# Optimization experiments

Measured on AMD Instinct MI355X. Metric: run time of the kernel, lower is better.

## Reference

```python
import jax, jax.numpy as jnp
import numpy as np

N = 100000
E = 6400000
D = 512


def setup_inputs() -> dict:
    key = jax.random.key(0)
    k1, k2, k3, k4 = jax.random.split(key, 4)
    x = jax.random.normal(k1, (N, D), dtype=jnp.float32)
    edge_index = jax.random.randint(k2, (2, E), 0, N, dtype=jnp.int64)
    edge_attr = jax.random.uniform(k3, (E,), dtype=jnp.float32)
    # xavier_normal_ on (in_feat, 1) with gain=1.414: std = gain*sqrt(2/(fan_in+fan_out))
    std = 1.414 * np.sqrt(2.0 / (D + 1))
    p = jax.random.normal(k4, (D, 1), dtype=jnp.float32) * std
    b = jnp.zeros((1,), dtype=jnp.float32)
    return {"x": x, "edge_index": edge_index, "edge_attr": edge_attr, "p": p, "b": b}


def reference(x, edge_index, edge_attr, p, b):
    # Per-node gate: sigmoid(x @ p + b), shape [N]
    diag_val = jax.nn.sigmoid(jnp.matmul(x, p) + b).reshape(-1)
    # spspmm(A, diag(d)) scales each edge value by d[col] = d[edge_index[1]]
    adj_mat_val = edge_attr * diag_val[edge_index[1]]
    return edge_index, adj_mat_val
```

## Files before the change

kernel.cpp:

```cpp
#include <hip/hip_runtime.h>
#include <math.h>


typedef float vf4 __attribute__((ext_vector_type(4)));
typedef int   vi4 __attribute__((ext_vector_type(4)));

__global__ __launch_bounds__(256) void gate_kernel(
    const float* __restrict__ x,
    const float* __restrict__ p,
    const float* __restrict__ b,
    float* __restrict__ gate,
    int N)
{
    const int wave_id = (blockIdx.x * blockDim.x + threadIdx.x) >> 6;
    const int lane    = threadIdx.x & 63;
    const float bb = b[0];

    const vf4* pr = (const vf4*)p;
    const vf4 p0 = pr[lane];
    const vf4 p1 = pr[lane + 64];

    const int row0 = wave_id * 4;
    if (row0 >= N) return;

    if (row0 + 3 < N) {
        const vf4* xr = (const vf4*)(x + (size_t)row0 * 512);
        vf4 a0 = __builtin_nontemporal_load(xr + lane);
        vf4 a1 = __builtin_nontemporal_load(xr + lane + 64);
        vf4 b0 = __builtin_nontemporal_load(xr + lane + 128);
        vf4 b1 = __builtin_nontemporal_load(xr + lane + 192);
        vf4 c0 = __builtin_nontemporal_load(xr + lane + 256);
        vf4 c1 = __builtin_nontemporal_load(xr + lane + 320);
        vf4 d0 = __builtin_nontemporal_load(xr + lane + 384);
        vf4 d1 = __builtin_nontemporal_load(xr + lane + 448);

        float s0 = a0.x * p0.x + a0.y * p0.y + a0.z * p0.z + a0.w * p0.w
                 + a1.x * p1.x + a1.y * p1.y + a1.z * p1.z + a1.w * p1.w;
        float s1 = b0.x * p0.x + b0.y * p0.y + b0.z * p0.z + b0.w * p0.w
                 + b1.x * p1.x + b1.y * p1.y + b1.z * p1.z + b1.w * p1.w;
        float s2 = c0.x * p0.x + c0.y * p0.y + c0.z * p0.z + c0.w * p0.w
                 + c1.x * p1.x + c1.y * p1.y + c1.z * p1.z + c1.w * p1.w;
        float s3 = d0.x * p0.x + d0.y * p0.y + d0.z * p0.z + d0.w * p0.w
                 + d1.x * p1.x + d1.y * p1.y + d1.z * p1.z + d1.w * p1.w;

        #pragma unroll
        for (int off = 32; off > 0; off >>= 1) {
            s0 += __shfl_down(s0, off, 64);
            s1 += __shfl_down(s1, off, 64);
            s2 += __shfl_down(s2, off, 64);
            s3 += __shfl_down(s3, off, 64);
        }
        if (lane == 0) {
            vf4 g;
            g.x = 1.0f / (1.0f + __expf(-(s0 + bb)));
            g.y = 1.0f / (1.0f + __expf(-(s1 + bb)));
            g.z = 1.0f / (1.0f + __expf(-(s2 + bb)));
            g.w = 1.0f / (1.0f + __expf(-(s3 + bb)));
            *(vf4*)(gate + row0) = g;
        }
    } else {
        for (int row = row0; row < N; ++row) {
            const vf4* xr = (const vf4*)(x + (size_t)row * 512);
            vf4 x0 = xr[lane];
            vf4 x1 = xr[lane + 64];
            float s = x0.x * p0.x + x0.y * p0.y + x0.z * p0.z + x0.w * p0.w
                    + x1.x * p1.x + x1.y * p1.y + x1.z * p1.z + x1.w * p1.w;
            #pragma unroll
            for (int off = 32; off > 0; off >>= 1)
                s += __shfl_down(s, off, 64);
            if (lane == 0)
                gate[row] = 1.0f / (1.0f + __expf(-(s + bb)));
        }
    }
}

__global__ __launch_bounds__(256) void edge_kernel(
    const int*   __restrict__ edge_index,
    const float* __restrict__ edge_attr,
    const float* __restrict__ gate,
    float* __restrict__ out,
    int E)
{
    const int tid = blockIdx.x * blockDim.x + threadIdx.x;
    const int EV4 = E >> 2;
    const int q0  = tid * 2;
    if (q0 >= EV4) return;

    const vi4* row4 = (const vi4*)edge_index;
    const vi4* col4 = (const vi4*)(edge_index + E);
    const vf4* ea4  = (const vf4*)edge_attr;

    vf4* outR = (vf4*)out;
    vf4* outC = (vf4*)(out + (size_t)E);
    vf4* outV = (vf4*)(out + 2 * (size_t)E);

    vi4 c0 = __builtin_nontemporal_load(col4 + q0);
    vi4 c1 = __builtin_nontemporal_load(col4 + q0 + 1);
    vi4 r0 = __builtin_nontemporal_load(row4 + q0);
    vi4 r1 = __builtin_nontemporal_load(row4 + q0 + 1);
    vf4 a0 = __builtin_nontemporal_load(ea4 + q0);
    vf4 a1 = __builtin_nontemporal_load(ea4 + q0 + 1);

    float g0x = gate[c0.x], g0y = gate[c0.y], g0z = gate[c0.z], g0w = gate[c0.w];
    float g1x = gate[c1.x], g1y = gate[c1.y], g1z = gate[c1.z], g1w = gate[c1.w];

    vf4 fr0; fr0.x = (float)r0.x; fr0.y = (float)r0.y; fr0.z = (float)r0.z; fr0.w = (float)r0.w;
    vf4 fr1; fr1.x = (float)r1.x; fr1.y = (float)r1.y; fr1.z = (float)r1.z; fr1.w = (float)r1.w;
    vf4 fc0; fc0.x = (float)c0.x; fc0.y = (float)c0.y; fc0.z = (float)c0.z; fc0.w = (float)c0.w;
    vf4 fc1; fc1.x = (float)c1.x; fc1.y = (float)c1.y; fc1.z = (float)c1.z; fc1.w = (float)c1.w;

    __builtin_nontemporal_store(fr0, outR + q0);
    __builtin_nontemporal_store(fr1, outR + q0 + 1);
    __builtin_nontemporal_store(fc0, outC + q0);
    __builtin_nontemporal_store(fc1, outC + q0 + 1);

    vf4 v0, v1;
    v0.x = a0.x * g0x;  v0.y = a0.y * g0y;  v0.z = a0.z * g0z;  v0.w = a0.w * g0w;
    v1.x = a1.x * g1x;  v1.y = a1.y * g1y;  v1.z = a1.z * g1z;  v1.w = a1.w * g1w;
    __builtin_nontemporal_store(v0, outV + q0);
    __builtin_nontemporal_store(v1, outV + q0 + 1);
}

extern "C" void kernel_launch(void* const* d_in, const int* in_sizes, int n_in,
                              void* d_out, int out_size, void* d_ws, size_t ws_size,
                              hipStream_t stream) {
    const float* x          = (const float*)d_in[0];
    const int*   edge_index = (const int*)  d_in[1];
    const float* edge_attr  = (const float*)d_in[2];
    const float* p          = (const float*)d_in[3];
    const float* b          = (const float*)d_in[4];

    const int D = in_sizes[3];
    const int N = in_sizes[0] / D;
    const int E = in_sizes[2];

    float* gate = (float*)d_ws;
    float* out  = (float*)d_out;

    int gate_waves  = (N + 3) / 4;
    int gate_blocks = (gate_waves + 3) / 4;
    gate_kernel<<<gate_blocks, 256, 0, stream>>>(x, p, b, gate, N);

    int edge_threads = (E >> 2) / 2;
    int edge_blocks  = (edge_threads + 255) / 256;
    edge_kernel<<<edge_blocks, 256, 0, stream>>>(edge_index, edge_attr, gate, out, E);
}
```

Before: 351.3 us.

## Fuse gate and edge kernels into one cooperative kernel with grid sync

```diff
diff --git a/kernel.cpp b/kernel.cpp
--- a/kernel.cpp
+++ b/kernel.cpp
@@ -1,28 +1,145 @@
 #include <hip/hip_runtime.h>
+#include <hip/hip_cooperative_groups.h>
 #include <math.h>
+
+namespace cg = cooperative_groups;
 
 
 typedef float vf4 __attribute__((ext_vector_type(4)));
 typedef int   vi4 __attribute__((ext_vector_type(4)));
 
-__global__ __launch_bounds__(256) void gate_kernel(
+#define COOP_BLOCKS 1024
+#define COOP_THREADS 256
+
+__global__ __launch_bounds__(256, 4) void fused_kernel(
     const float* __restrict__ x,
+    const int*   __restrict__ edge_index,
+    const float* __restrict__ edge_attr,
     const float* __restrict__ p,
     const float* __restrict__ b,
     float* __restrict__ gate,
-    int N)
+    float* __restrict__ out,
+    int N, int E)
+{
+    const int tid     = blockIdx.x * blockDim.x + threadIdx.x;
+    const int nthread = gridDim.x * blockDim.x;
+    const int wave_id = tid >> 6;
+    const int lane    = threadIdx.x & 63;
+    const int nwaves  = nthread >> 6;
+
+    const int EV4 = E >> 2;
+
+    {
+        const vi4* row4 = (const vi4*)edge_index;
+        vf4*       outR = (vf4*)out;
+        for (int i = tid; i < EV4; i += nthread) {
+            vi4 r = __builtin_nontemporal_load(row4 + i);
+            vf4 fr;
+            fr.x = (float)r.x; fr.y = (float)r.y;
+            fr.z = (float)r.z; fr.w = (float)r.w;
+            __builtin_nontemporal_store(fr, outR + i);
+        }
+    }
+
+    {
+        const float bb = b[0];
+        const vf4* pr = (const vf4*)p;
+        const vf4 p0 = pr[lane];
+        const vf4 p1 = pr[lane + 64];
+        const int ntask = (N + 3) >> 2;
+
+        for (int t = wave_id; t < ntask; t += nwaves) {
+            const int row0 = t * 4;
+            if (row0 + 3 < N) {
+                const vf4* xr = (const vf4*)(x + (size_t)row0 * 512);
+                vf4 a0 = __builtin_nontemporal_load(xr + lane);
+                vf4 a1 = __builtin_nontemporal_load(xr + lane + 64);
+                vf4 b0 = __builtin_nontemporal_load(xr + lane + 128);
+                vf4 b1 = __builtin_nontemporal_load(xr + lane + 192);
+                vf4 c0 = __builtin_nontemporal_load(xr + lane + 256);
+                vf4 c1 = __builtin_nontemporal_load(xr + lane + 320);
+                vf4 d0 = __builtin_nontemporal_load(xr + lane + 384);
+                vf4 d1 = __builtin_nontemporal_load(xr + lane + 448);
+
+                float s0 = a0.x*p0.x + a0.y*p0.y + a0.z*p0.z + a0.w*p0.w
+                         + a1.x*p1.x + a1.y*p1.y + a1.z*p1.z + a1.w*p1.w;
+                float s1 = b0.x*p0.x + b0.y*p0.y + b0.z*p0.z + b0.w*p0.w
+                         + b1.x*p1.x + b1.y*p1.y + b1.z*p1.z + b1.w*p1.w;
+                float s2 = c0.x*p0.x + c0.y*p0.y + c0.z*p0.z + c0.w*p0.w
+                         + c1.x*p1.x + c1.y*p1.y + c1.z*p1.z + c1.w*p1.w;
+                float s3 = d0.x*p0.x + d0.y*p0.y + d0.z*p0.z + d0.w*p0.w
+                         + d1.x*p1.x + d1.y*p1.y + d1.z*p1.z + d1.w*p1.w;
+
+                #pragma unroll
+                for (int off = 32; off > 0; off >>= 1) {
+                    s0 += __shfl_down(s0, off, 64);
+                    s1 += __shfl_down(s1, off, 64);
+                    s2 += __shfl_down(s2, off, 64);
+                    s3 += __shfl_down(s3, off, 64);
+                }
+                if (lane == 0) {
+                    vf4 g;
+                    g.x = 1.0f / (1.0f + __expf(-(s0 + bb)));
+                    g.y = 1.0f / (1.0f + __expf(-(s1 + bb)));
+                    g.z = 1.0f / (1.0f + __expf(-(s2 + bb)));
+                    g.w = 1.0f / (1.0f + __expf(-(s3 + bb)));
+                    *(vf4*)(gate + row0) = g;
+                }
+            } else {
+                for (int row = row0; row < N; ++row) {
+                    const vf4* xr = (const vf4*)(x + (size_t)row * 512);
+                    vf4 x0 = xr[lane];
+                    vf4 x1 = xr[lane + 64];
+                    float s = x0.x*p0.x + x0.y*p0.y + x0.z*p0.z + x0.w*p0.w
+                            + x1.x*p1.x + x1.y*p1.y + x1.z*p1.z + x1.w*p1.w;
+                    #pragma unroll
+                    for (int off = 32; off > 0; off >>= 1)
+                        s += __shfl_down(s, off, 64);
+                    if (lane == 0)
+                        gate[row] = 1.0f / (1.0f + __expf(-(s + bb)));
+                }
+            }
+        }
+    }
+
+    cg::this_grid().sync();
+
+    {
+        const vi4* col4 = (const vi4*)(edge_index + E);
+        const vf4* ea4  = (const vf4*)edge_attr;
+        vf4* outC = (vf4*)(out + (size_t)E);
+        vf4* outV = (vf4*)(out + 2 * (size_t)E);
+
+        for (int i = tid; i < EV4; i += nthread) {
+            vi4 c = __builtin_nontemporal_load(col4 + i);
+            vf4 a = __builtin_nontemporal_load(ea4 + i);
+
+            float gx = gate[c.x], gy = gate[c.y], gz = gate[c.z], gw = gate[c.w];
+
+            vf4 fc;
+            fc.x = (float)c.x; fc.y = (float)c.y;
+            fc.z = (float)c.z; fc.w = (float)c.w;
+            __builtin_nontemporal_store(fc, outC + i);
+
+            vf4 v;
+            v.x = a.x * gx; v.y = a.y * gy; v.z = a.z * gz; v.w = a.w * gw;
+            __builtin_nontemporal_store(v, outV + i);
+        }
+    }
+}
+
+__global__ __launch_bounds__(256) void gate_kernel(
+    const float* __restrict__ x, const float* __restrict__ p,
+    const float* __restrict__ b, float* __restrict__ gate, int N)
 {
     const int wave_id = (blockIdx.x * blockDim.x + threadIdx.x) >> 6;
     const int lane    = threadIdx.x & 63;
     const float bb = b[0];
-
     const vf4* pr = (const vf4*)p;
     const vf4 p0 = pr[lane];
     const vf4 p1 = pr[lane + 64];
-
     const int row0 = wave_id * 4;
     if (row0 >= N) return;
-
     if (row0 + 3 < N) {
         const vf4* xr = (const vf4*)(x + (size_t)row0 * 512);
         vf4 a0 = __builtin_nontemporal_load(xr + lane);
@@ -33,16 +150,14 @@
         vf4 c1 = __builtin_nontemporal_load(xr + lane + 320);
         vf4 d0 = __builtin_nontemporal_load(xr + lane + 384);
         vf4 d1 = __builtin_nontemporal_load(xr + lane + 448);
-
-        float s0 = a0.x * p0.x + a0.y * p0.y + a0.z * p0.z + a0.w * p0.w
-                 + a1.x * p1.x + a1.y * p1.y + a1.z * p1.z + a1.w * p1.w;
-        float s1 = b0.x * p0.x + b0.y * p0.y + b0.z * p0.z + b0.w * p0.w
-                 + b1.x * p1.x + b1.y * p1.y + b1.z * p1.z + b1.w * p1.w;
-        float s2 = c0.x * p0.x + c0.y * p0.y + c0.z * p0.z + c0.w * p0.w
-                 + c1.x * p1.x + c1.y * p1.y + c1.z * p1.z + c1.w * p1.w;
-        float s3 = d0.x * p0.x + d0.y * p0.y + d0.z * p0.z + d0.w * p0.w
-                 + d1.x * p1.x + d1.y * p1.y + d1.z * p1.z + d1.w * p1.w;
-
+        float s0 = a0.x*p0.x + a0.y*p0.y + a0.z*p0.z + a0.w*p0.w
+                 + a1.x*p1.x + a1.y*p1.y + a1.z*p1.z + a1.w*p1.w;
+        float s1 = b0.x*p0.x + b0.y*p0.y + b0.z*p0.z + b0.w*p0.w
+                 + b1.x*p1.x + b1.y*p1.y + b1.z*p1.z + b1.w*p1.w;
+        float s2 = c0.x*p0.x + c0.y*p0.y + c0.z*p0.z + c0.w*p0.w
+                 + c1.x*p1.x + c1.y*p1.y + c1.z*p1.z + c1.w*p1.w;
+        float s3 = d0.x*p0.x + d0.y*p0.y + d0.z*p0.z + d0.w*p0.w
+                 + d1.x*p1.x + d1.y*p1.y + d1.z*p1.z + d1.w*p1.w;
         #pragma unroll
         for (int off = 32; off > 0; off >>= 1) {
             s0 += __shfl_down(s0, off, 64);
@@ -63,8 +178,8 @@
             const vf4* xr = (const vf4*)(x + (size_t)row * 512);
             vf4 x0 = xr[lane];
             vf4 x1 = xr[lane + 64];
-            float s = x0.x * p0.x + x0.y * p0.y + x0.z * p0.z + x0.w * p0.w
-                    + x1.x * p1.x + x1.y * p1.y + x1.z * p1.z + x1.w * p1.w;
+            float s = x0.x*p0.x + x0.y*p0.y + x0.z*p0.z + x0.w*p0.w
+                    + x1.x*p1.x + x1.y*p1.y + x1.z*p1.z + x1.w*p1.w;
             #pragma unroll
             for (int off = 32; off > 0; off >>= 1)
                 s += __shfl_down(s, off, 64);
@@ -75,48 +190,38 @@
 }
 
 __global__ __launch_bounds__(256) void edge_kernel(
-    const int*   __restrict__ edge_index,
-    const float* __restrict__ edge_attr,
-    const float* __restrict__ gate,
-    float* __restrict__ out,
-    int E)
+    const int* __restrict__ edge_index, const float* __restrict__ edge_attr,
+    const float* __restrict__ gate, float* __restrict__ out, int E)
 {
     const int tid = blockIdx.x * blockDim.x + threadIdx.x;
     const int EV4 = E >> 2;
     const int q0  = tid * 2;
     if (q0 >= EV4) return;
-
     const vi4* row4 = (const vi4*)edge_index;
     const vi4* col4 = (const vi4*)(edge_index + E);
     const vf4* ea4  = (const vf4*)edge_attr;
-
     vf4* outR = (vf4*)out;
     vf4* outC = (vf4*)(out + (size_t)E);
     vf4* outV = (vf4*)(out + 2 * (size_t)E);
-
     vi4 c0 = __builtin_nontemporal_load(col4 + q0);
     vi4 c1 = __builtin_nontemporal_load(col4 + q0 + 1);
     vi4 r0 = __builtin_nontemporal_load(row4 + q0);
     vi4 r1 = __builtin_nontemporal_load(row4 + q0 + 1);
     vf4 a0 = __builtin_nontemporal_load(ea4 + q0);
     vf4 a1 = __builtin_nontemporal_load(ea4 + q0 + 1);
-
     float g0x = gate[c0.x], g0y = gate[c0.y], g0z = gate[c0.z], g0w = gate[c0.w];
     float g1x = gate[c1.x], g1y = gate[c1.y], g1z = gate[c1.z], g1w = gate[c1.w];
-
-    vf4 fr0; fr0.x = (float)r0.x; fr0.y = (float)r0.y; fr0.z = (float)r0.z; fr0.w = (float)r0.w;
-    vf4 fr1; fr1.x = (float)r1.x; fr1.y = (float)r1.y; fr1.z = (float)r1.z; fr1.w = (float)r1.w;
-    vf4 fc0; fc0.x = (float)c0.x; fc0.y = (float)c0.y; fc0.z = (float)c0.z; fc0.w = (float)c0.w;
-    vf4 fc1; fc1.x = (float)c1.x; fc1.y = (float)c1.y; fc1.z = (float)c1.z; fc1.w = (float)c1.w;
-
+    vf4 fr0; fr0.x=(float)r0.x; fr0.y=(float)r0.y; fr0.z=(float)r0.z; fr0.w=(float)r0.w;
+    vf4 fr1; fr1.x=(float)r1.x; fr1.y=(float)r1.y; fr1.z=(float)r1.z; fr1.w=(float)r1.w;
+    vf4 fc0; fc0.x=(float)c0.x; fc0.y=(float)c0.y; fc0.z=(float)c0.z; fc0.w=(float)c0.w;
+    vf4 fc1; fc1.x=(float)c1.x; fc1.y=(float)c1.y; fc1.z=(float)c1.z; fc1.w=(float)c1.w;
     __builtin_nontemporal_store(fr0, outR + q0);
     __builtin_nontemporal_store(fr1, outR + q0 + 1);
     __builtin_nontemporal_store(fc0, outC + q0);
     __builtin_nontemporal_store(fc1, outC + q0 + 1);
-
     vf4 v0, v1;
-    v0.x = a0.x * g0x;  v0.y = a0.y * g0y;  v0.z = a0.z * g0z;  v0.w = a0.w * g0w;
-    v1.x = a1.x * g1x;  v1.y = a1.y * g1y;  v1.z = a1.z * g1z;  v1.w = a1.w * g1w;
+    v0.x = a0.x*g0x; v0.y = a0.y*g0y; v0.z = a0.z*g0z; v0.w = a0.w*g0w;
+    v1.x = a1.x*g1x; v1.y = a1.y*g1y; v1.z = a1.z*g1z; v1.w = a1.w*g1w;
     __builtin_nontemporal_store(v0, outV + q0);
     __builtin_nontemporal_store(v1, outV + q0 + 1);
 }
@@ -131,17 +236,25 @@
     const float* b          = (const float*)d_in[4];
 
     const int D = in_sizes[3];
-    const int N = in_sizes[0] / D;
-    const int E = in_sizes[2];
+    int N = in_sizes[0] / D;
+    int E = in_sizes[2];
 
     float* gate = (float*)d_ws;
     float* out  = (float*)d_out;
 
-    int gate_waves  = (N + 3) / 4;
-    int gate_blocks = (gate_waves + 3) / 4;
-    gate_kernel<<<gate_blocks, 256, 0, stream>>>(x, p, b, gate, N);
-
-    int edge_threads = (E >> 2) / 2;
-    int edge_blocks  = (edge_threads + 255) / 256;
-    edge_kernel<<<edge_blocks, 256, 0, stream>>>(edge_index, edge_attr, gate, out, E);
-}
+    void* args[] = {(void*)&x, (void*)&edge_index, (void*)&edge_attr,
+                    (void*)&p, (void*)&b, (void*)&gate, (void*)&out,
+                    (void*)&N, (void*)&E};
+    hipError_t err = hipLaunchCooperativeKernel(
+        (const void*)fused_kernel, dim3(COOP_BLOCKS), dim3(COOP_THREADS),
+        args, 0, stream);
+
+    if (err != hipSuccess) {
+        int gate_waves  = (N + 3) / 4;
+        int gate_blocks = (gate_waves + 3) / 4;
+        gate_kernel<<<gate_blocks, 256, 0, stream>>>(x, p, b, gate, N);
+        int edge_threads = (E >> 2) / 2;
+        int edge_blocks  = (edge_threads + 255) / 256;
+        edge_kernel<<<edge_blocks, 256, 0, stream>>>(edge_index, edge_attr, gate, out, E);
+    }
+}
```

Result: slower. 487.1 us (+38.6%).

## Move row-index conversion into gate kernel to overlap with gate GEMV

Applied to the files above, without the earlier changes.

```diff
diff --git a/kernel.cpp b/kernel.cpp
--- a/kernel.cpp
+++ b/kernel.cpp
@@ -5,72 +5,94 @@
 typedef float vf4 __attribute__((ext_vector_type(4)));
 typedef int   vi4 __attribute__((ext_vector_type(4)));
 
-__global__ __launch_bounds__(256) void gate_kernel(
+__global__ __launch_bounds__(256) void gate_rowconv_kernel(
     const float* __restrict__ x,
+    const int*   __restrict__ edge_index,
     const float* __restrict__ p,
     const float* __restrict__ b,
     float* __restrict__ gate,
-    int N)
+    float* __restrict__ out,
+    int N, int E, int gate_blocks)
 {
-    const int wave_id = (blockIdx.x * blockDim.x + threadIdx.x) >> 6;
-    const int lane    = threadIdx.x & 63;
-    const float bb = b[0];
+    if ((int)blockIdx.x < gate_blocks) {
+        const int wave_id = (blockIdx.x * blockDim.x + threadIdx.x) >> 6;
+        const int lane    = threadIdx.x & 63;
+        const float bb = b[0];
 
-    const vf4* pr = (const vf4*)p;
-    const vf4 p0 = pr[lane];
-    const vf4 p1 = pr[lane + 64];
+        const vf4* pr = (const vf4*)p;
+        const vf4 p0 = pr[lane];
+        const vf4 p1 = pr[lane + 64];
 
-    const int row0 = wave_id * 4;
-    if (row0 >= N) return;
+        const int row0 = wave_id * 4;
+        if (row0 >= N) return;
 
-    if (row0 + 3 < N) {
-        const vf4* xr = (const vf4*)(x + (size_t)row0 * 512);
-        vf4 a0 = __builtin_nontemporal_load(xr + lane);
-        vf4 a1 = __builtin_nontemporal_load(xr + lane + 64);
-        vf4 b0 = __builtin_nontemporal_load(xr + lane + 128);
-        vf4 b1 = __builtin_nontemporal_load(xr + lane + 192);
-        vf4 c0 = __builtin_nontemporal_load(xr + lane + 256);
-        vf4 c1 = __builtin_nontemporal_load(xr + lane + 320);
-        vf4 d0 = __builtin_nontemporal_load(xr + lane + 384);
-        vf4 d1 = __builtin_nontemporal_load(xr + lane + 448);
+        if (row0 + 3 < N) {
+            const vf4* xr = (const vf4*)(x + (size_t)row0 * 512);
+            vf4 a0 = __builtin_nontemporal_load(xr + lane);
+            vf4 a1 = __builtin_nontemporal_load(xr + lane + 64);
+            vf4 b0 = __builtin_nontemporal_load(xr + lane + 128);
+            vf4 b1 = __builtin_nontemporal_load(xr + lane + 192);
+            vf4 c0 = __builtin_nontemporal_load(xr + lane + 256);
+            vf4 c1 = __builtin_nontemporal_load(xr + lane + 320);
+            vf4 d0 = __builtin_nontemporal_load(xr + lane + 384);
+            vf4 d1 = __builtin_nontemporal_load(xr + lane + 448);
 
-        float s0 = a0.x * p0.x + a0.y * p0.y + a0.z * p0.z + a0.w * p0.w
-                 + a1.x * p1.x + a1.y * p1.y + a1.z * p1.z + a1.w * p1.w;
-        float s1 = b0.x * p0.x + b0.y * p0.y + b0.z * p0.z + b0.w * p0.w
-                 + b1.x * p1.x + b1.y * p1.y + b1.z * p1.z + b1.w * p1.w;
-        float s2 = c0.x * p0.x + c0.y * p0.y + c0.z * p0.z + c0.w * p0.w
-                 + c1.x * p1.x + c1.y * p1.y + c1.z * p1.z + c1.w * p1.w;
-        float s3 = d0.x * p0.x + d0.y * p0.y + d0.z * p0.z + d0.w * p0.w
-                 + d1.x * p1.x + d1.y * p1.y + d1.z * p1.z + d1.w * p1.w;
+            float s0 = a0.x*p0.x + a0.y*p0.y + a0.z*p0.z + a0.w*p0.w
+                     + a1.x*p1.x + a1.y*p1.y + a1.z*p1.z + a1.w*p1.w;
+            float s1 = b0.x*p0.x + b0.y*p0.y + b0.z*p0.z + b0.w*p0.w
+                     + b1.x*p1.x + b1.y*p1.y + b1.z*p1.z + b1.w*p1.w;
+            float s2 = c0.x*p0.x + c0.y*p0.y + c0.z*p0.z + c0.w*p0.w
+                     + c1.x*p1.x + c1.y*p1.y + c1.z*p1.z + c1.w*p1.w;
+            float s3 = d0.x*p0.x + d0.y*p0.y + d0.z*p0.z + d0.w*p0.w
+                     + d1.x*p1.x + d1.y*p1.y + d1.z*p1.z + d1.w*p1.w;
 
-        #pragma unroll
-        for (int off = 32; off > 0; off >>= 1) {
-            s0 += __shfl_down(s0, off, 64);
-            s1 += __shfl_down(s1, off, 64);
-            s2 += __shfl_down(s2, off, 64);
-            s3 += __shfl_down(s3, off, 64);
-        }
-        if (lane == 0) {
-            vf4 g;
-            g.x = 1.0f / (1.0f + __expf(-(s0 + bb)));
-            g.y = 1.0f / (1.0f + __expf(-(s1 + bb)));
-            g.z = 1.0f / (1.0f + __expf(-(s2 + bb)));
-            g.w = 1.0f / (1.0f + __expf(-(s3 + bb)));
-            *(vf4*)(gate + row0) = g;
+            #pragma unroll
+            for (int off = 32; off > 0; off >>= 1) {
+                s0 += __shfl_down(s0, off, 64);
+                s1 += __shfl_down(s1, off, 64);
+                s2 += __shfl_down(s2, off, 64);
+                s3 += __shfl_down(s3, off, 64);
+            }
+            if (lane == 0) {
+                vf4 g;
+                g.x = 1.0f / (1.0f + __expf(-(s0 + bb)));
+                g.y = 1.0f / (1.0f + __expf(-(s1 + bb)));
+                g.z = 1.0f / (1.0f + __expf(-(s2 + bb)));
+                g.w = 1.0f / (1.0f + __expf(-(s3 + bb)));
+                *(vf4*)(gate + row0) = g;
+            }
+        } else {
+            for (int row = row0; row < N; ++row) {
+                const vf4* xr = (const vf4*)(x + (size_t)row * 512);
+                vf4 x0 = xr[lane];
+                vf4 x1 = xr[lane + 64];
+                float s = x0.x*p0.x + x0.y*p0.y + x0.z*p0.z + x0.w*p0.w
+                        + x1.x*p1.x + x1.y*p1.y + x1.z*p1.z + x1.w*p1.w;
+                #pragma unroll
+                for (int off = 32; off > 0; off >>= 1)
+                    s += __shfl_down(s, off, 64);
+                if (lane == 0)
+                    gate[row] = 1.0f / (1.0f + __expf(-(s + bb)));
+            }
         }
     } else {
-        for (int row = row0; row < N; ++row) {
-            const vf4* xr = (const vf4*)(x + (size_t)row * 512);
-            vf4 x0 = xr[lane];
-            vf4 x1 = xr[lane + 64];
-            float s = x0.x * p0.x + x0.y * p0.y + x0.z * p0.z + x0.w * p0.w
-                    + x1.x * p1.x + x1.y * p1.y + x1.z * p1.z + x1.w * p1.w;
-            #pragma unroll
-            for (int off = 32; off > 0; off >>= 1)
-                s += __shfl_down(s, off, 64);
-            if (lane == 0)
-                gate[row] = 1.0f / (1.0f + __expf(-(s + bb)));
-        }
+        const int tid = ((int)blockIdx.x - gate_blocks) * blockDim.x + threadIdx.x;
+        const int EV4 = E >> 2;
+        const int q0  = tid * 2;
+        if (q0 >= EV4) return;
+
+        const vi4* row4 = (const vi4*)edge_index;
+        vf4*       outR = (vf4*)out;
+
+        vi4 r0 = __builtin_nontemporal_load(row4 + q0);
+        vi4 r1 = __builtin_nontemporal_load(row4 + q0 + 1);
+
+        vf4 fr0; fr0.x=(float)r0.x; fr0.y=(float)r0.y; fr0.z=(float)r0.z; fr0.w=(float)r0.w;
+        vf4 fr1; fr1.x=(float)r1.x; fr1.y=(float)r1.y; fr1.z=(float)r1.z; fr1.w=(float)r1.w;
+
+        __builtin_nontemporal_store(fr0, outR + q0);
+        if (q0 + 1 < EV4)
+            __builtin_nontemporal_store(fr1, outR + q0 + 1);
     }
 }
 
@@ -86,37 +108,29 @@
     const int q0  = tid * 2;
     if (q0 >= EV4) return;
 
-    const vi4* row4 = (const vi4*)edge_index;
     const vi4* col4 = (const vi4*)(edge_index + E);
     const vf4* ea4  = (const vf4*)edge_attr;
 
-    vf4* outR = (vf4*)out;
     vf4* outC = (vf4*)(out + (size_t)E);
     vf4* outV = (vf4*)(out + 2 * (size_t)E);
 
     vi4 c0 = __builtin_nontemporal_load(col4 + q0);
     vi4 c1 = __builtin_nontemporal_load(col4 + q0 + 1);
-    vi4 r0 = __builtin_nontemporal_load(row4 + q0);
-    vi4 r1 = __builtin_nontemporal_load(row4 + q0 + 1);
     vf4 a0 = __builtin_nontemporal_load(ea4 + q0);
     vf4 a1 = __builtin_nontemporal_load(ea4 + q0 + 1);
 
     float g0x = gate[c0.x], g0y = gate[c0.y], g0z = gate[c0.z], g0w = gate[c0.w];
     float g1x = gate[c1.x], g1y = gate[c1.y], g1z = gate[c1.z], g1w = gate[c1.w];
 
-    vf4 fr0; fr0.x = (float)r0.x; fr0.y = (float)r0.y; fr0.z = (float)r0.z; fr0.w = (float)r0.w;
-    vf4 fr1; fr1.x = (float)r1.x; fr1.y = (float)r1.y; fr1.z = (float)r1.z; fr1.w = (float)r1.w;
-    vf4 fc0; fc0.x = (float)c0.x; fc0.y = (float)c0.y; fc0.z = (float)c0.z; fc0.w = (float)c0.w;
-    vf4 fc1; fc1.x = (float)c1.x; fc1.y = (float)c1.y; fc1.z = (float)c1.z; fc1.w = (float)c1.w;
+    vf4 fc0; fc0.x=(float)c0.x; fc0.y=(float)c0.y; fc0.z=(float)c0.z; fc0.w=(float)c0.w;
+    vf4 fc1; fc1.x=(float)c1.x; fc1.y=(float)c1.y; fc1.z=(float)c1.z; fc1.w=(float)c1.w;
 
-    __builtin_nontemporal_store(fr0, outR + q0);
-    __builtin_nontemporal_store(fr1, outR + q0 + 1);
     __builtin_nontemporal_store(fc0, outC + q0);
     __builtin_nontemporal_store(fc1, outC + q0 + 1);
 
     vf4 v0, v1;
-    v0.x = a0.x * g0x;  v0.y = a0.y * g0y;  v0.z = a0.z * g0z;  v0.w = a0.w * g0w;
-    v1.x = a1.x * g1x;  v1.y = a1.y * g1y;  v1.z = a1.z * g1z;  v1.w = a1.w * g1w;
+    v0.x = a0.x*g0x; v0.y = a0.y*g0y; v0.z = a0.z*g0z; v0.w = a0.w*g0w;
+    v1.x = a1.x*g1x; v1.y = a1.y*g1y; v1.z = a1.z*g1z; v1.w = a1.w*g1w;
     __builtin_nontemporal_store(v0, outV + q0);
     __builtin_nontemporal_store(v1, outV + q0 + 1);
 }
@@ -131,17 +145,20 @@
     const float* b          = (const float*)d_in[4];
 
     const int D = in_sizes[3];
-    const int N = in_sizes[0] / D;
-    const int E = in_sizes[2];
+    int N = in_sizes[0] / D;
+    int E = in_sizes[2];
 
     float* gate = (float*)d_ws;
     float* out  = (float*)d_out;
 
     int gate_waves  = (N + 3) / 4;
     int gate_blocks = (gate_waves + 3) / 4;
-    gate_kernel<<<gate_blocks, 256, 0, stream>>>(x, p, b, gate, N);
+    int conv_threads = ((E >> 2) + 1) / 2;
+    int conv_blocks  = (conv_threads + 255) / 256;
+    gate_rowconv_kernel<<<gate_blocks + conv_blocks, 256, 0, stream>>>(
+        x, edge_index, p, b, gate, out, N, E, gate_blocks);
 
-    int edge_threads = (E >> 2) / 2;
+    int edge_threads = ((E >> 2) + 1) / 2;
     int edge_blocks  = (edge_threads + 255) / 256;
     edge_kernel<<<edge_blocks, 256, 0, stream>>>(edge_index, edge_attr, gate, out, E);
 }
```

Measured after the change: 357.2 us. No clear change (+1.7%).
